# Optimization experiments

Hardware: AMD Instinct MI355X
Metric: run time of the kernel (lower is better)

The kernel has to match this reference:

```python
import jax, jax.numpy as jnp
import numpy as np

N = 10000
E = 160000
IN_DIM = 128
HID = 128
HEADS = 8
INT_DIM = 512
OUT_DIM = 3
NEG_SLOPE = 0.2


def gat_conv(x, src, dst, W, a_src, a_dst, b, heads, ch):
    # x: [N, F_in]; W: [F_in, heads*ch]; a_src/a_dst: [heads, ch]; b: [heads*ch]
    n = x.shape[0]
    h = (x @ W).reshape(n, heads, ch)                      # [N,H,C]
    alpha_src = jnp.einsum('nhc,hc->nh', h, a_src)         # [N,H]
    alpha_dst = jnp.einsum('nhc,hc->nh', h, a_dst)         # [N,H]
    e = jax.nn.leaky_relu(alpha_src[src] + alpha_dst[dst], NEG_SLOPE)  # [E,H]
    # segment softmax over incoming edges of each dst node
    emax = jax.ops.segment_max(e, dst, num_segments=n)     # [N,H]
    ee = jnp.exp(e - emax[dst])
    denom = jax.ops.segment_sum(ee, dst, num_segments=n)   # [N,H]
    alpha = ee / (denom[dst] + 1e-16)                      # [E,H]
    msg = h[src] * alpha[:, :, None]                       # [E,H,C]
    out = jax.ops.segment_sum(msg, dst, num_segments=n)    # [N,H,C]
    return out.reshape(n, heads * ch) + b


def setup_inputs() -> dict:
    key = jax.random.key(0)
    ks = jax.random.split(key, 20)

    def glorot(k, shape):
        fan = shape[0] + shape[-1]
        s = jnp.sqrt(6.0 / fan)
        return jax.random.uniform(k, shape, jnp.float32, -s, s)

    x = jax.random.normal(ks[0], (N, IN_DIM), jnp.float32)
    edge_index = jax.random.randint(ks[1], (2, E), 0, N, jnp.int32)
    return {
        'x': x,
        'edge_index': edge_index,
        'W1': glorot(ks[2], (IN_DIM, HEADS * HID)),
        'a_src1': glorot(ks[3], (HEADS, HID)),
        'a_dst1': glorot(ks[4], (HEADS, HID)),
        'b1': jnp.zeros((HEADS * HID,), jnp.float32),
        'W2': glorot(ks[5], (HEADS * HID, HEADS * HID)),
        'a_src2': glorot(ks[6], (HEADS, HID)),
        'a_dst2': glorot(ks[7], (HEADS, HID)),
        'b2': jnp.zeros((HEADS * HID,), jnp.float32),
        'W3': glorot(ks[8], (HEADS * HID, INT_DIM)),
        'a_src3': glorot(ks[9], (1, INT_DIM)),
        'a_dst3': glorot(ks[10], (1, INT_DIM)),
        'b3': jnp.zeros((INT_DIM,), jnp.float32),
        'Wl': glorot(ks[11], (INT_DIM, INT_DIM)),
        'bl': jnp.zeros((INT_DIM,), jnp.float32),
        'Wc': glorot(ks[12], (INT_DIM, OUT_DIM)),
        'bc': jnp.zeros((OUT_DIM,), jnp.float32),
    }


def reference(x, edge_index, W1, a_src1, a_dst1, b1, W2, a_src2, a_dst2, b2,
              W3, a_src3, a_dst3, b3, Wl, bl, Wc, bc):
    src, dst = edge_index[0], edge_index[1]
    # eval mode: dropout_edge and Dropout are identity
    h = gat_conv(x, src, dst, W1, a_src1, a_dst1, b1, HEADS, HID)
    h = jax.nn.relu(h)
    h = gat_conv(h, src, dst, W2, a_src2, a_dst2, b2, HEADS, HID)
    h = jax.nn.relu(h)
    h = gat_conv(h, src, dst, W3, a_src3, a_dst3, b3, 1, INT_DIM)
    h = jax.nn.relu(h)
    h = jax.nn.relu(h @ Wl + bl)
    return h @ Wc + bc
```

## Files before the change

kernel.cpp:

```cpp
#include <hip/hip_runtime.h>
#include <hip/hip_bf16.h>

#define NN 10000
#define EE 160000
#define IN_DIM 128
#define HID 128
#define HEADS 8
#define F1 (HEADS*HID)
#define INT_DIM 512
#define OUT_DIM 3
#define MPAD 10112

typedef __attribute__((ext_vector_type(4))) float f32x4;
typedef __attribute__((ext_vector_type(8))) _Float16 half8;
typedef __attribute__((ext_vector_type(4))) _Float16 half4;
typedef __attribute__((ext_vector_type(2))) _Float16 half2v;

#define WAVE_SYNC() do { asm volatile("s_waitcnt lgkmcnt(0)" ::: "memory"); \
                         __builtin_amdgcn_sched_barrier(0); } while(0)

#define FMA_MIX_LO(acc, pair, w) asm("v_fma_mix_f32 %0, %1, %2, %0 op_sel:[0,0,0] op_sel_hi:[1,0,0]" \
                                     : "+v"(acc) : "v"(pair), "v"(w))
#define FMA_MIX_HI(acc, pair, w) asm("v_fma_mix_f32 %0, %1, %2, %0 op_sel:[1,0,0] op_sel_hi:[1,0,0]" \
                                     : "+v"(acc) : "v"(pair), "v"(w))

__device__ inline void fma_mix8(float* acc, uint4 v, float w){
    FMA_MIX_LO(acc[0], v.x, w);  FMA_MIX_HI(acc[1], v.x, w);
    FMA_MIX_LO(acc[2], v.y, w);  FMA_MIX_HI(acc[3], v.y, w);
    FMA_MIX_LO(acc[4], v.z, w);  FMA_MIX_HI(acc[5], v.z, w);
    FMA_MIX_LO(acc[6], v.w, w);  FMA_MIX_HI(acc[7], v.w, w);
}

__global__ __launch_bounds__(1024) void scan_kernel(const int* __restrict__ cnt, int* __restrict__ rowp,
                                                    int* __restrict__ cursor, int n){
    int t = threadIdx.x;
    int base = t*10;
    int vals[10];
    int run = 0;
    #pragma unroll
    for(int k=0;k<10;k++){
        int i = base+k;
        int v = (i<n) ? cnt[i] : 0;
        vals[k] = run;
        run += v;
    }
    int lane = t & 63, wv = t >> 6;
    int inc = run;
    #pragma unroll
    for(int off=1; off<64; off<<=1){
        int u = __shfl_up(inc, off);
        if(lane >= off) inc += u;
    }
    __shared__ int wtot[16], woff[16];
    if(lane == 63) wtot[wv] = inc;
    __syncthreads();
    if(t < 16){
        int v = wtot[t];
        int inc2 = v;
        #pragma unroll
        for(int off=1; off<16; off<<=1){
            int u = __shfl_up(inc2, off);
            if(t >= off) inc2 += u;
        }
        woff[t] = inc2 - v;
    }
    __syncthreads();
    int thread_excl = woff[wv] + inc - run;
    #pragma unroll
    for(int k=0;k<10;k++){
        int i = base+k;
        if(i<n){
            int v = thread_excl + vals[k];
            rowp[i] = v;
            cursor[i] = v;
        }
    }
    if(t == 1023) rowp[n] = thread_excl + run;
}

__global__ __launch_bounds__(256) void fill_kernel(const int* __restrict__ src, const int* __restrict__ dst,
                                                   int E, int* __restrict__ cursor, int* __restrict__ colsrc){
    int e = blockIdx.x*256 + threadIdx.x;
    if(e < E){
        int d = dst[e];
        int pos = atomicAdd(&cursor[d], 1);
        colsrc[pos] = src[e];
    }
}

__device__ inline void transpose_tile16(const float* __restrict__ B, _Float16* __restrict__ T,
                                        int K, int N, int idx){
    __shared__ float tile[32][33];
    const int tx = threadIdx.x & 31, ty = threadIdx.x >> 5;
    const int gx = N >> 5;
    const int n0 = (idx % gx) * 32, k0 = (idx / gx) * 32;
    #pragma unroll
    for(int i = 0; i < 32; i += 8)
        tile[ty + i][tx] = B[(size_t)(k0 + ty + i) * N + n0 + tx];
    __syncthreads();
    #pragma unroll
    for(int i = 0; i < 32; i += 8){
        int nn = ty + i;
        T[(size_t)(n0 + nn) * K + k0 + tx] = (_Float16)tile[tx][nn];
    }
}

__global__ __launch_bounds__(256) void prep_kernel(
    const float* __restrict__ W1, const float* __restrict__ W2,
    const float* __restrict__ W3, const float* __restrict__ Wl,
    const float* __restrict__ x,
    const float* __restrict__ a_src1, const float* __restrict__ a_dst1,
    _Float16* __restrict__ tW1, _Float16* __restrict__ tW2,
    _Float16* __restrict__ tW3, _Float16* __restrict__ tWl,
    _Float16* __restrict__ x16, float* __restrict__ aw,
    int* __restrict__ cnt)
{
    int b = blockIdx.x;
    if(b < 128){            transpose_tile16(W1, tW1, IN_DIM, F1, b); }
    else if(b < 1152){      transpose_tile16(W2, tW2, F1, F1, b-128); }
    else if(b < 1664){      transpose_tile16(W3, tW3, F1, INT_DIM, b-1152); }
    else if(b < 1920){      transpose_tile16(Wl, tWl, INT_DIM, INT_DIM, b-1664); }
    else if(b < 3170){
        int i = (b-1920)*256 + threadIdx.x;
        float4 v = ((const float4*)x)[i];
        half4 o = { (_Float16)v.x, (_Float16)v.y, (_Float16)v.z, (_Float16)v.w };
        ((half4*)x16)[i] = o;
    }
    else if(b < 3178){
        int idx = (b-3170)*256 + threadIdx.x;
        if(idx < 16*IN_DIM){
            int j = idx >> 7, k = idx & 127;
            int hj = j & 7;
            const float* av = (j < 8 ? a_src1 : a_dst1) + hj*HID;
            const float* wr = W1 + (size_t)k*F1 + hj*HID;
            float s = 0.f;
            #pragma unroll 4
            for(int c = 0; c < HID; c++) s += av[c] * wr[c];
            aw[idx] = s;
        }
    }
    else {
        int i = (b-3178)*1024 + threadIdx.x*4;
        if(i < NN) *(int4*)(cnt + i) = (int4){0,0,0,0};
    }
}

__global__ __launch_bounds__(256) void count_alpha1_kernel(
    const int* __restrict__ dst, int* __restrict__ cnt,
    const float* __restrict__ x, const float* __restrict__ aw,
    float* __restrict__ asrc, float* __restrict__ adst)
{
    int b = blockIdx.x;
    if(b < 625){
        int e = b*256 + threadIdx.x;
        if(e < EE) atomicAdd(&cnt[dst[e]], 1);
        return;
    }
    __shared__ float xs[16][128];
    __shared__ float aws[16][128];
    int t = threadIdx.x;
    int nb = (b - 625) * 16;
    for(int i = t; i < 16*128; i += 256){
        xs[i >> 7][i & 127] = x[(size_t)nb*128 + i];
        aws[i >> 7][i & 127] = aw[i];
    }
    __syncthreads();
    int nl = t >> 4, j = t & 15;
    float s = 0.f;
    #pragma unroll 4
    for(int c = 0; c < 128; c++) s += xs[nl][c] * aws[j][c];
    int node = nb + nl;
    if(j < 8) asrc[node*8 + j] = s;
    else      adst[node*8 + (j-8)] = s;
}

__global__ __launch_bounds__(256) void agg1_kernel(const _Float16* __restrict__ x16,
                                                   const float* __restrict__ asrc,
                                                   const float* __restrict__ adst,
                                                   const int* __restrict__ rowp,
                                                   const int* __restrict__ colsrc,
                                                   _Float16* __restrict__ oa){
    const int w = threadIdx.x >> 6, l = threadIdx.x & 63;
    const int node = blockIdx.x*4 + w;
    __shared__ float sh_ee[4][64][8];
    int beg = rowp[node], end = rowp[node+1];
    float rd = adst[node*8 + (l & 7)];
    float acc0[8], acc1[8];
    #pragma unroll
    for(int h=0;h<8;h++){ acc0[h]=0.f; acc1[h]=0.f; }
    float dpart = 0.f;
    const char* xb = (const char*)x16 + 4*l;
    for(int base=beg; base<end; base+=64){
        int clen = min(64, end-base);
        WAVE_SYNC();
        unsigned soff = 0;
        if(l < clen) soff = (unsigned)colsrc[base + l] << 8;
        for(int it=l; it<clen*8; it+=64){
            int j = it >> 3;
            int s = colsrc[base + j];
            float e = asrc[s*8 + (l & 7)] + rd;
            e = (e > 0.f) ? e : 0.2f*e;
            float ee = expf(e);
            sh_ee[w][j][l & 7] = ee;
            dpart += ee;
        }
        WAVE_SYNC();
        #pragma unroll 2
        for(int j=0;j<clen;j++){
            unsigned o = (unsigned)__shfl((int)soff, j);
            unsigned pair = *(const unsigned*)(xb + o);
            #pragma unroll
            for(int h=0;h<8;h++){
                float wt = sh_ee[w][j][h];
                FMA_MIX_LO(acc0[h], pair, wt);
                FMA_MIX_HI(acc1[h], pair, wt);
            }
        }
    }
    dpart += __shfl_xor(dpart, 8);
    dpart += __shfl_xor(dpart, 16);
    dpart += __shfl_xor(dpart, 32);
    #pragma unroll
    for(int h=0;h<8;h++){
        float dn = __shfl(dpart, h) + 1e-16f;
        half2v o = { (_Float16)(acc0[h]/dn), (_Float16)(acc1[h]/dn) };
        *(half2v*)(oa + (size_t)node*F1 + h*128 + 2*l) = o;
    }
}

__device__ inline void agg_gather(const char* hb, unsigned soff, float ee, int clen,
                                  int g, uint4 v0, float w0, float* acc){
    int cpad = (clen + 3) & ~3;
    #pragma unroll 1
    for(int j0=0; j0<cpad; j0+=4){
        uint4 nv; float nw = 0.f;
        const bool more = (j0+4 < cpad);
        if(more){
            unsigned no = (unsigned)__shfl((int)soff, j0+4+g);
            nw = __shfl(ee, j0+4+g);
            nv = *(const uint4*)(hb + no);
        }
        fma_mix8(acc, v0, w0);
        if(more){ v0 = nv; w0 = nw; }
    }
}

__device__ inline void agg2_chunk(const char* hb, const float* asrc, const int* colsrc,
                                  int base, int clen, float rd, int h, int l, int g,
                                  float* acc, float& dpart){
    unsigned soff = 0; float eereg = 0.f;
    if(l < clen){
        int s = colsrc[base + l];
        soff = (unsigned)s << 11;
        float e = asrc[s*8 + h] + rd;
        e = (e > 0.f) ? e : 0.2f*e;
        eereg = expf(e);
        dpart += eereg;
    }
    unsigned o0 = (unsigned)__shfl((int)soff, g);
    float w0 = __shfl(eereg, g);
    uint4 v0 = *(const uint4*)(hb + o0);
    agg_gather(hb, soff, eereg, clen, g, v0, w0, acc);
}

__device__ inline void agg3_chunk(const char* hb, const float* asrc, const int* colsrc,
                                  int base, int clen, float rd, int l, int g,
                                  float* acc, float& dpart){
    unsigned soff = 0; float eereg = 0.f;
    if(l < clen){
        int s = colsrc[base + l];
        soff = (unsigned)s << 10;
        float e = asrc[s] + rd;
        e = (e > 0.f) ? e : 0.2f*e;
        eereg = expf(e);
        dpart += eereg;
    }
    unsigned o0 = (unsigned)__shfl((int)soff, g);
    float w0 = __shfl(eereg, g);
    uint4 v0 = *(const uint4*)(hb + o0);
    agg_gather(hb, soff, eereg, clen, g, v0, w0, acc);
}

__global__ __launch_bounds__(256) void agg2_kernel(const _Float16* __restrict__ hbuf,
                                                   const float* __restrict__ asrc,
                                                   const float* __restrict__ adst,
                                                   const int* __restrict__ rowp,
                                                   const int* __restrict__ colsrc,
                                                   const float* __restrict__ bias,
                                                   _Float16* __restrict__ oa){
    const int w = threadIdx.x >> 6, l = threadIdx.x & 63;
    const int h = blockIdx.x & 7;
    const int nA = (blockIdx.x >> 3)*8 + w*2;
    const int nB = nA + 1;
    const int g = l >> 4, i = l & 15;
    const char* hb = (const char*)hbuf + h*256 + 16*i;

    int begA = rowp[nA], endA = rowp[nA+1];
    int begB = rowp[nB], endB = rowp[nB+1];
    float rdA = adst[nA*8 + h];
    float rdB = adst[nB*8 + h];
    int clenA = min(64, endA - begA);
    int clenB = min(64, endB - begB);
    int sA = (l < clenA) ? colsrc[begA + l] : 0;
    int sB = (l < clenB) ? colsrc[begB + l] : 0;
    unsigned soffA = 0, soffB = 0;
    float eeA = 0.f, eeB = 0.f;
    if(l < clenA){
        soffA = (unsigned)sA << 11;
        float e = asrc[sA*8 + h] + rdA;
        e = (e > 0.f) ? e : 0.2f*e;
        eeA = expf(e);
    }
    if(l < clenB){
        soffB = (unsigned)sB << 11;
        float e = asrc[sB*8 + h] + rdB;
        e = (e > 0.f) ? e : 0.2f*e;
        eeB = expf(e);
    }
    unsigned oA = (unsigned)__shfl((int)soffA, g);
    float wA = __shfl(eeA, g);
    uint4 vA = *(const uint4*)(hb + oA);
    unsigned oB = (unsigned)__shfl((int)soffB, g);
    float wB = __shfl(eeB, g);
    uint4 vB = *(const uint4*)(hb + oB);

    float accA[8];
    #pragma unroll
    for(int k=0;k<8;k++) accA[k]=0.f;
    float dpA = eeA;
    agg_gather(hb, soffA, eeA, clenA, g, vA, wA, accA);
    for(int base=begA+64; base<endA; base+=64)
        agg2_chunk(hb, asrc, colsrc, base, min(64, endA-base), rdA, h, l, g, accA, dpA);

    float accB[8];
    #pragma unroll
    for(int k=0;k<8;k++) accB[k]=0.f;
    float dpB = eeB;
    agg_gather(hb, soffB, eeB, clenB, g, vB, wB, accB);
    for(int base=begB+64; base<endB; base+=64)
        agg2_chunk(hb, asrc, colsrc, base, min(64, endB-base), rdB, h, l, g, accB, dpB);

    #pragma unroll
    for(int k=0;k<8;k++){
        accA[k] += __shfl_xor(accA[k], 16);
        accA[k] += __shfl_xor(accA[k], 32);
        accB[k] += __shfl_xor(accB[k], 16);
        accB[k] += __shfl_xor(accB[k], 32);
    }
    #pragma unroll
    for(int off=1; off<64; off<<=1){
        dpA += __shfl_xor(dpA, off);
        dpB += __shfl_xor(dpB, off);
    }
    if(g == 0){
        const int f = h*128 + 8*i;
        float4 b0 = *(const float4*)(bias + f);
        float4 b1 = *(const float4*)(bias + f + 4);
        float bb[8] = {b0.x,b0.y,b0.z,b0.w, b1.x,b1.y,b1.z,b1.w};
        float dnA = dpA + 1e-16f, dnB = dpB + 1e-16f;
        half8 oA8, oB8;
        #pragma unroll
        for(int k=0;k<8;k++){
            oA8[k] = (_Float16)fmaxf(accA[k]/dnA + bb[k], 0.f);
            oB8[k] = (_Float16)fmaxf(accB[k]/dnB + bb[k], 0.f);
        }
        *(half8*)(oa + (size_t)nA*F1 + f) = oA8;
        *(half8*)(oa + (size_t)nB*F1 + f) = oB8;
    }
}

__global__ __launch_bounds__(256) void agg3_kernel(const _Float16* __restrict__ hbuf,
                                                   const float* __restrict__ asrc,
                                                   const float* __restrict__ adst,
                                                   const int* __restrict__ rowp,
                                                   const int* __restrict__ colsrc,
                                                   const float* __restrict__ bias,
                                                   _Float16* __restrict__ oa){
    const int w = threadIdx.x >> 6, l = threadIdx.x & 63;
    const int i7 = blockIdx.x & 7;
    const int chunk = i7 & 3, sub = i7 >> 2;
    const int nA = ((blockIdx.x >> 3)*2 + sub)*8 + w*2;
    const int nB = nA + 1;
    const int g = l >> 4, i = l & 15;
    const char* hb = (const char*)hbuf + chunk*256 + 16*i;

    int begA = rowp[nA], endA = rowp[nA+1];
    int begB = rowp[nB], endB = rowp[nB+1];
    float rdA = adst[nA];
    float rdB = adst[nB];
    int clenA = min(64, endA - begA);
    int clenB = min(64, endB - begB);
    int sA = (l < clenA) ? colsrc[begA + l] : 0;
    int sB = (l < clenB) ? colsrc[begB + l] : 0;
    unsigned soffA = 0, soffB = 0;
    float eeA = 0.f, eeB = 0.f;
    if(l < clenA){
        soffA = (unsigned)sA << 10;
        float e = asrc[sA] + rdA;
        e = (e > 0.f) ? e : 0.2f*e;
        eeA = expf(e);
    }
    if(l < clenB){
        soffB = (unsigned)sB << 10;
        float e = asrc[sB] + rdB;
        e = (e > 0.f) ? e : 0.2f*e;
        eeB = expf(e);
    }
    unsigned oA = (unsigned)__shfl((int)soffA, g);
    float wA = __shfl(eeA, g);
    uint4 vA = *(const uint4*)(hb + oA);
    unsigned oB = (unsigned)__shfl((int)soffB, g);
    float wB = __shfl(eeB, g);
    uint4 vB = *(const uint4*)(hb + oB);

    float accA[8];
    #pragma unroll
    for(int k=0;k<8;k++) accA[k]=0.f;
    float dpA = eeA;
    agg_gather(hb, soffA, eeA, clenA, g, vA, wA, accA);
    for(int base=begA+64; base<endA; base+=64)
        agg3_chunk(hb, asrc, colsrc, base, min(64, endA-base), rdA, l, g, accA, dpA);

    float accB[8];
    #pragma unroll
    for(int k=0;k<8;k++) accB[k]=0.f;
    float dpB = eeB;
    agg_gather(hb, soffB, eeB, clenB, g, vB, wB, accB);
    for(int base=begB+64; base<endB; base+=64)
        agg3_chunk(hb, asrc, colsrc, base, min(64, endB-base), rdB, l, g, accB, dpB);

    #pragma unroll
    for(int k=0;k<8;k++){
        accA[k] += __shfl_xor(accA[k], 16);
        accA[k] += __shfl_xor(accA[k], 32);
        accB[k] += __shfl_xor(accB[k], 16);
        accB[k] += __shfl_xor(accB[k], 32);
    }
    #pragma unroll
    for(int off=1; off<64; off<<=1){
        dpA += __shfl_xor(dpA, off);
        dpB += __shfl_xor(dpB, off);
    }
    if(g == 0){
        const int f = chunk*128 + 8*i;
        float4 b0 = *(const float4*)(bias + f);
        float4 b1 = *(const float4*)(bias + f + 4);
        float bb[8] = {b0.x,b0.y,b0.z,b0.w, b1.x,b1.y,b1.z,b1.w};
        float dnA = dpA + 1e-16f, dnB = dpB + 1e-16f;
        half8 oA8, oB8;
        #pragma unroll
        for(int k=0;k<8;k++){
            oA8[k] = (_Float16)fmaxf(accA[k]/dnA + bb[k], 0.f);
            oB8[k] = (_Float16)fmaxf(accB[k]/dnB + bb[k], 0.f);
        }
        *(half8*)(oa + (size_t)nA*INT_DIM + f) = oA8;
        *(half8*)(oa + (size_t)nB*INT_DIM + f) = oB8;
    }
}

template<int FUSE>
__global__ __launch_bounds__(512, 4) void mfma16_gemm_kernel(
    const _Float16* __restrict__ A, int lda, int za,
    const _Float16* __restrict__ B, int ldb, int zb,
    const float* __restrict__ bias, _Float16* __restrict__ O,
    int ldc, int zc, int K, int gx)
{
    __shared__ _Float16 lA[2][128*32];
    __shared__ _Float16 lB[2][128*32];
    const int tid  = threadIdx.x;
    const int lane = tid & 63;
    const int w    = tid >> 6;
    const int wm   = w >> 2;
    const int wn   = w & 3;
    const int z    = blockIdx.z;

    const int nwg = gridDim.x;
    const int q = nwg >> 3, r = nwg & 7;
    const int xcd = blockIdx.x & 7, idx = blockIdx.x >> 3;
    const int wgid = (xcd < r ? xcd*(q+1) : r*(q+1) + (xcd-r)*q) + idx;
    const int row0 = (wgid / gx) * 128, col0 = (wgid % gx) * 128;

    f32x4 acc[4][2];
    #pragma unroll
    for(int i=0;i<4;i++)
        #pragma unroll
        for(int j=0;j<2;j++) acc[i][j] = (f32x4){0.f,0.f,0.f,0.f};

    const int rr1 = tid >> 2;
    const int ss1 = (tid & 3) ^ ((rr1 >> 1) & 3);
    const size_t aoff = (size_t)(row0 + rr1) * lda + (size_t)z*za + ss1 * 8;
    const size_t boff = (size_t)(col0 + rr1) * ldb + (size_t)z*zb + ss1 * 8;

    typedef __attribute__((address_space(3))) char lds_char;
    lds_char* dA = (lds_char*)(&lA[0][0]) + w*1024;
    lds_char* dB = (lds_char*)(&lB[0][0]) + w*1024;

    int arow[4], brow[2];
    const int slotx = ((lane >> 4) ^ ((lane >> 1) & 3)) << 4;
    #pragma unroll
    for(int i=0;i<4;i++)
        arow[i] = (wm*64 + i*16 + (lane & 15)) * 64 + slotx;
    #pragma unroll
    for(int j=0;j<2;j++)
        brow[j] = (wn*32 + j*16 + (lane & 15)) * 64 + slotx;

    #define GLDS(src, dst) __builtin_amdgcn_global_load_lds( \
        (__attribute__((address_space(1))) void*)(src), \
        (__attribute__((address_space(3))) void*)(dst), 16, 0, 0)
    GLDS(A + aoff, dA);
    GLDS(B + boff, dB);
    __syncthreads();

    #pragma unroll 1
    for(int k0 = 0, kb = 0; k0 < K; k0 += 32, kb ^= 1){
        if(k0 + 32 < K){
            const int nb = kb ^ 1;
            GLDS(A + aoff + k0 + 32, dA + nb*8192);
            GLDS(B + boff + k0 + 32, dB + nb*8192);
        }
        const char* pA = (const char*)(&lA[0][0]) + kb*8192;
        const char* pB = (const char*)(&lB[0][0]) + kb*8192;
        half8 af[4];
        #pragma unroll
        for(int i=0;i<4;i++) af[i] = *(const half8*)(pA + arow[i]);
        #pragma unroll
        for(int j=0;j<2;j++){
            half8 bf = *(const half8*)(pB + brow[j]);
            #pragma unroll
            for(int i=0;i<4;i++)
                acc[i][j] = __builtin_amdgcn_mfma_f32_16x16x32_f16(af[i], bf, acc[i][j], 0, 0, 0);
        }
        __syncthreads();
    }
    #undef GLDS

    #pragma unroll
    for(int i=0;i<4;i++){
        const int rr = row0 + wm*64 + i*16 + ((lane >> 4) << 2);
        #pragma unroll
        for(int j=0;j<2;j++){
            const int gc = z*zc + col0 + wn*32 + j*16 + (lane & 15);
            float b = FUSE ? bias[gc] : 0.f;
            #pragma unroll
            for(int rg=0;rg<4;rg++){
                float v = acc[i][j][rg];
                if(FUSE) v = fmaxf(v + b, 0.f);
                O[(size_t)(rr + rg) * ldc + gc] = (_Float16)v;
            }
        }
    }
}

__global__ __launch_bounds__(128) void alpha16_h8_kernel(const _Float16* __restrict__ hbuf,
                                                         const float* __restrict__ a_src,
                                                         const float* __restrict__ a_dst,
                                                         float* __restrict__ asrc, float* __restrict__ adst){
    int node = blockIdx.x;
    int t = threadIdx.x;
    half8 v = ((const half8*)(hbuf + (size_t)node*F1))[t];
    const float4* ap = (const float4*)(a_src + 8*t);
    const float4* dp = (const float4*)(a_dst + 8*t);
    float4 a0 = ap[0], a1 = ap[1];
    float4 d0 = dp[0], d1 = dp[1];
    float av[8] = {a0.x,a0.y,a0.z,a0.w, a1.x,a1.y,a1.z,a1.w};
    float dv[8] = {d0.x,d0.y,d0.z,d0.w, d1.x,d1.y,d1.z,d1.w};
    float ps = 0.f, pd = 0.f;
    #pragma unroll
    for(int k=0;k<8;k++){
        float f = (float)v[k];
        ps += f * av[k];
        pd += f * dv[k];
    }
    #pragma unroll
    for(int off=8; off; off>>=1){ ps += __shfl_down(ps, off); pd += __shfl_down(pd, off); }
    if((t & 15) == 0){
        asrc[(size_t)node*8 + (t>>4)] = ps;
        adst[(size_t)node*8 + (t>>4)] = pd;
    }
}

__global__ __launch_bounds__(128) void alpha16_h1_kernel(const _Float16* __restrict__ hbuf,
                                                         const float* __restrict__ a_src,
                                                         const float* __restrict__ a_dst,
                                                         float* __restrict__ asrc, float* __restrict__ adst){
    int node = blockIdx.x;
    int t = threadIdx.x;
    half4 v = ((const half4*)(hbuf + (size_t)node*INT_DIM))[t];
    float4 a = ((const float4*)a_src)[t];
    float4 d = ((const float4*)a_dst)[t];
    float ps = (float)v[0]*a.x + (float)v[1]*a.y + (float)v[2]*a.z + (float)v[3]*a.w;
    float pd = (float)v[0]*d.x + (float)v[1]*d.y + (float)v[2]*d.z + (float)v[3]*d.w;
    #pragma unroll
    for(int off=32; off; off>>=1){ ps += __shfl_down(ps, off); pd += __shfl_down(pd, off); }
    __shared__ float shs[2], shd[2];
    int wv = t >> 6;
    if((t & 63) == 0){ shs[wv] = ps; shd[wv] = pd; }
    __syncthreads();
    if(t == 0){
        asrc[node] = shs[0] + shs[1];
        adst[node] = shd[0] + shd[1];
    }
}

__global__ __launch_bounds__(256) void cls16_kernel(const _Float16* __restrict__ h, const float* __restrict__ Wc,
                                                    const float* __restrict__ bc, float* __restrict__ out, int n){
    int node = blockIdx.x*4 + (threadIdx.x >> 6);
    int lane = threadIdx.x & 63;
    if(node >= n) return;
    half8 v = ((const half8*)(h + (size_t)node*INT_DIM))[lane];
    float s0=0.f, s1=0.f, s2=0.f;
    #pragma unroll
    for(int k=0;k<8;k++){
        float f = (float)v[k];
        const float* wr = Wc + (8*lane + k)*3;
        s0 += f * wr[0];
        s1 += f * wr[1];
        s2 += f * wr[2];
    }
    #pragma unroll
    for(int off=32; off; off>>=1){
        s0 += __shfl_down(s0, off);
        s1 += __shfl_down(s1, off);
        s2 += __shfl_down(s2, off);
    }
    if(lane==0){
        out[(size_t)node*3+0] = s0 + bc[0];
        out[(size_t)node*3+1] = s1 + bc[1];
        out[(size_t)node*3+2] = s2 + bc[2];
    }
}

extern "C" void kernel_launch(void* const* d_in, const int* in_sizes, int n_in,
                              void* d_out, int out_size, void* d_ws, size_t ws_size,
                              hipStream_t stream){
    const float* x      = (const float*)d_in[0];
    const int*   ei     = (const int*)d_in[1];
    const float* W1     = (const float*)d_in[2];
    const float* a_src1 = (const float*)d_in[3];
    const float* a_dst1 = (const float*)d_in[4];
    const float* b1     = (const float*)d_in[5];
    const float* W2     = (const float*)d_in[6];
    const float* a_src2 = (const float*)d_in[7];
    const float* a_dst2 = (const float*)d_in[8];
    const float* b2     = (const float*)d_in[9];
    const float* W3     = (const float*)d_in[10];
    const float* a_src3 = (const float*)d_in[11];
    const float* a_dst3 = (const float*)d_in[12];
    const float* b3     = (const float*)d_in[13];
    const float* Wl     = (const float*)d_in[14];
    const float* bl     = (const float*)d_in[15];
    const float* Wc     = (const float*)d_in[16];
    const float* bc     = (const float*)d_in[17];
    float* out = (float*)d_out;

    const int* src = ei;
    const int* dst = ei + EE;

    char* p = (char*)d_ws;
    char* regA = p;  p += (size_t)MPAD*F1*4;
    char* regB = p;  p += (size_t)MPAD*F1*4;
    float* aw1  = (float*)p;  p += 16*IN_DIM*4;
    float* asrc = (float*)p;  p += (size_t)NN*HEADS*4;
    float* adst = (float*)p;  p += (size_t)NN*HEADS*4;
    int* cnt    = (int*)p;    p += NN*4;
    int* rowp   = (int*)p;    p += (NN+1)*4;
    int* cursor = (int*)p;    p += NN*4;
    int* colsrc = (int*)p;    p += EE*4;

    _Float16* hA = (_Float16*)regA;
    _Float16* hB = (_Float16*)regB;
    _Float16* up   = (_Float16*)(regA + (size_t)MPAD*F1*2);
    _Float16* tW1  = up;
    _Float16* tW2  = tW1 + (size_t)F1*IN_DIM;
    _Float16* tW3  = tW2 + (size_t)F1*F1;
    _Float16* tWl  = tW3 + (size_t)INT_DIM*F1;
    _Float16* x16  = tWl + (size_t)INT_DIM*INT_DIM;

    prep_kernel<<<3188, 256, 0, stream>>>(W1, W2, W3, Wl, x, a_src1, a_dst1,
                                          tW1, tW2, tW3, tWl, x16, aw1, cnt);
    count_alpha1_kernel<<<1250, 256, 0, stream>>>(dst, cnt, x, aw1, asrc, adst);
    scan_kernel<<<1, 1024, 0, stream>>>(cnt, rowp, cursor, NN);
    fill_kernel<<<(EE+255)/256, 256, 0, stream>>>(src, dst, EE, cursor, colsrc);

    agg1_kernel<<<NN/4, 256, 0, stream>>>(x16, asrc, adst, rowp, colsrc, hA);
    mfma16_gemm_kernel<1><<<dim3(MPAD/128, 1, HEADS), 512, 0, stream>>>(
        hA, F1, 128,  tW1, IN_DIM, 128*IN_DIM,
        b1, hB, F1, 128,  IN_DIM, 1);

    mfma16_gemm_kernel<0><<<dim3((F1/128)*(MPAD/128), 1, 1), 512, 0, stream>>>(
        hB, F1, 0,  tW2, F1, 0,
        nullptr, hA, F1, 0,  F1, F1/128);
    alpha16_h8_kernel<<<NN, 128, 0, stream>>>(hA, a_src2, a_dst2, asrc, adst);
    agg2_kernel<<<(NN/8)*8, 256, 0, stream>>>(hA, asrc, adst, rowp, colsrc, b2, hB);

    mfma16_gemm_kernel<0><<<dim3((INT_DIM/128)*(MPAD/128), 1, 1), 512, 0, stream>>>(
        hB, F1, 0,  tW3, F1, 0,
        nullptr, hA, INT_DIM, 0,  F1, INT_DIM/128);
    alpha16_h1_kernel<<<NN, 128, 0, stream>>>(hA, a_src3, a_dst3, asrc, adst);
    agg3_kernel<<<(NN/16)*8, 256, 0, stream>>>(hA, asrc, adst, rowp, colsrc, b3, hB);

    mfma16_gemm_kernel<1><<<dim3((INT_DIM/128)*(MPAD/128), 1, 1), 512, 0, stream>>>(
        hB, INT_DIM, 0,  tWl, INT_DIM, 0,
        bl, hA, INT_DIM, 0,  INT_DIM, INT_DIM/128);

    cls16_kernel<<<(NN+3)/4, 256, 0, stream>>>(hA, Wc, bc, out, NN);
}
```

Measured before the change: 247.1 us.

## Rotate per-node head chunks in GEMM output to spread aggregation gathers across channels

The layer-2 and layer-3 GEMMs now write each node's 128-column head or chunk groups rotated by the node index. The alpha and aggregation kernels read through the same permutation. Concurrent blocks for the same head therefore touch different 256-byte offsets within rows, which should spread gather traffic across memory channels and banks and reduce hot-spotting. It adds a few integer ops per address and couples the producer and consumer layouts, so any mismatch would silently corrupt results.

```diff
diff --git a/kernel.cpp b/kernel.cpp
--- a/kernel.cpp
+++ b/kernel.cpp
@@ -251,7 +251,7 @@
     unsigned soff = 0; float eereg = 0.f;
     if(l < clen){
         int s = colsrc[base + l];
-        soff = (unsigned)s << 11;
+        soff = ((unsigned)s << 11) | ((unsigned)((h + s) & 7) << 8);
         float e = asrc[s*8 + h] + rd;
         e = (e > 0.f) ? e : 0.2f*e;
         eereg = expf(e);
@@ -264,12 +264,12 @@
 }
 
 __device__ inline void agg3_chunk(const char* hb, const float* asrc, const int* colsrc,
-                                  int base, int clen, float rd, int l, int g,
+                                  int base, int clen, float rd, int chunk, int l, int g,
                                   float* acc, float& dpart){
     unsigned soff = 0; float eereg = 0.f;
     if(l < clen){
         int s = colsrc[base + l];
-        soff = (unsigned)s << 10;
+        soff = ((unsigned)s << 10) | ((unsigned)((chunk + s) & 3) << 8);
         float e = asrc[s] + rd;
         e = (e > 0.f) ? e : 0.2f*e;
         eereg = expf(e);
@@ -293,7 +293,7 @@
     const int nA = (blockIdx.x >> 3)*8 + w*2;
     const int nB = nA + 1;
     const int g = l >> 4, i = l & 15;
-    const char* hb = (const char*)hbuf + h*256 + 16*i;
+    const char* hb = (const char*)hbuf + 16*i;
 
     int begA = rowp[nA], endA = rowp[nA+1];
     int begB = rowp[nB], endB = rowp[nB+1];
@@ -306,13 +306,13 @@
     unsigned soffA = 0, soffB = 0;
     float eeA = 0.f, eeB = 0.f;
     if(l < clenA){
-        soffA = (unsigned)sA << 11;
+        soffA = ((unsigned)sA << 11) | ((unsigned)((h + sA) & 7) << 8);
         float e = asrc[sA*8 + h] + rdA;
         e = (e > 0.f) ? e : 0.2f*e;
         eeA = expf(e);
     }
     if(l < clenB){
-        soffB = (unsigned)sB << 11;
+        soffB = ((unsigned)sB << 11) | ((unsigned)((h + sB) & 7) << 8);
         float e = asrc[sB*8 + h] + rdB;
         e = (e > 0.f) ? e : 0.2f*e;
         eeB = expf(e);
@@ -382,7 +382,7 @@
     const int nA = ((blockIdx.x >> 3)*2 + sub)*8 + w*2;
     const int nB = nA + 1;
     const int g = l >> 4, i = l & 15;
-    const char* hb = (const char*)hbuf + chunk*256 + 16*i;
+    const char* hb = (const char*)hbuf + 16*i;
 
     int begA = rowp[nA], endA = rowp[nA+1];
     int begB = rowp[nB], endB = rowp[nB+1];
@@ -395,13 +395,13 @@
     unsigned soffA = 0, soffB = 0;
     float eeA = 0.f, eeB = 0.f;
     if(l < clenA){
-        soffA = (unsigned)sA << 10;
+        soffA = ((unsigned)sA << 10) | ((unsigned)((chunk + sA) & 3) << 8);
         float e = asrc[sA] + rdA;
         e = (e > 0.f) ? e : 0.2f*e;
         eeA = expf(e);
     }
     if(l < clenB){
-        soffB = (unsigned)sB << 10;
+        soffB = ((unsigned)sB << 10) | ((unsigned)((chunk + sB) & 3) << 8);
         float e = asrc[sB] + rdB;
         e = (e > 0.f) ? e : 0.2f*e;
         eeB = expf(e);
@@ -419,7 +419,7 @@
     float dpA = eeA;
     agg_gather(hb, soffA, eeA, clenA, g, vA, wA, accA);
     for(int base=begA+64; base<endA; base+=64)
-        agg3_chunk(hb, asrc, colsrc, base, min(64, endA-base), rdA, l, g, accA, dpA);
+        agg3_chunk(hb, asrc, colsrc, base, min(64, endA-base), rdA, chunk, l, g, accA, dpA);
 
     float accB[8];
     #pragma unroll
@@ -427,7 +427,7 @@
     float dpB = eeB;
     agg_gather(hb, soffB, eeB, clenB, g, vB, wB, accB);
     for(int base=begB+64; base<endB; base+=64)
-        agg3_chunk(hb, asrc, colsrc, base, min(64, endB-base), rdB, l, g, accB, dpB);
+        agg3_chunk(hb, asrc, colsrc, base, min(64, endB-base), rdB, chunk, l, g, accB, dpB);
 
     #pragma unroll
     for(int k=0;k<8;k++){
@@ -458,7 +458,7 @@
     }
 }
 
-template<int FUSE>
+template<int FUSE, int ROTM>
 __global__ __launch_bounds__(512, 4) void mfma16_gemm_kernel(
     const _Float16* __restrict__ A, int lda, int za,
     const _Float16* __restrict__ B, int ldb, int zb,
@@ -545,7 +545,13 @@
             for(int rg=0;rg<4;rg++){
                 float v = acc[i][j][rg];
                 if(FUSE) v = fmaxf(v + b, 0.f);
-                O[(size_t)(rr + rg) * ldc + gc] = (_Float16)v;
+                const int node = rr + rg;
+                int pc = gc;
+                if(ROTM){
+                    int grp = ((gc >> 7) + node) & ROTM;
+                    pc = (gc & 127) | (grp << 7);
+                }
+                O[(size_t)node * ldc + pc] = (_Float16)v;
             }
         }
     }
@@ -557,7 +563,9 @@
                                                          float* __restrict__ asrc, float* __restrict__ adst){
     int node = blockIdx.x;
     int t = threadIdx.x;
-    half8 v = ((const half8*)(hbuf + (size_t)node*F1))[t];
+    int head = t >> 4;
+    int poff = (((head + node) & 7) << 7) + ((t & 15) << 3);
+    half8 v = *(const half8*)(hbuf + (size_t)node*F1 + poff);
     const float4* ap = (const float4*)(a_src + 8*t);
     const float4* dp = (const float4*)(a_dst + 8*t);
     float4 a0 = ap[0], a1 = ap[1];
@@ -574,8 +582,8 @@
     #pragma unroll
     for(int off=8; off; off>>=1){ ps += __shfl_down(ps, off); pd += __shfl_down(pd, off); }
     if((t & 15) == 0){
-        asrc[(size_t)node*8 + (t>>4)] = ps;
-        adst[(size_t)node*8 + (t>>4)] = pd;
+        asrc[(size_t)node*8 + head] = ps;
+        adst[(size_t)node*8 + head] = pd;
     }
 }
 
@@ -585,7 +593,9 @@
                                                          float* __restrict__ asrc, float* __restrict__ adst){
     int node = blockIdx.x;
     int t = threadIdx.x;
-    half4 v = ((const half4*)(hbuf + (size_t)node*INT_DIM))[t];
+    int chunk = t >> 5;
+    int poff = (((chunk + node) & 3) << 7) + ((t & 31) << 2);
+    half4 v = *(const half4*)(hbuf + (size_t)node*INT_DIM + poff);
     float4 a = ((const float4*)a_src)[t];
     float4 d = ((const float4*)a_dst)[t];
     float ps = (float)v[0]*a.x + (float)v[1]*a.y + (float)v[2]*a.z + (float)v[3]*a.w;
@@ -683,23 +693,23 @@
     fill_kernel<<<(EE+255)/256, 256, 0, stream>>>(src, dst, EE, cursor, colsrc);
 
     agg1_kernel<<<NN/4, 256, 0, stream>>>(x16, asrc, adst, rowp, colsrc, hA);
-    mfma16_gemm_kernel<1><<<dim3(MPAD/128, 1, HEADS), 512, 0, stream>>>(
+    mfma16_gemm_kernel<1,0><<<dim3(MPAD/128, 1, HEADS), 512, 0, stream>>>(
         hA, F1, 128,  tW1, IN_DIM, 128*IN_DIM,
         b1, hB, F1, 128,  IN_DIM, 1);
 
-    mfma16_gemm_kernel<0><<<dim3((F1/128)*(MPAD/128), 1, 1), 512, 0, stream>>>(
+    mfma16_gemm_kernel<0,7><<<dim3((F1/128)*(MPAD/128), 1, 1), 512, 0, stream>>>(
         hB, F1, 0,  tW2, F1, 0,
         nullptr, hA, F1, 0,  F1, F1/128);
     alpha16_h8_kernel<<<NN, 128, 0, stream>>>(hA, a_src2, a_dst2, asrc, adst);
     agg2_kernel<<<(NN/8)*8, 256, 0, stream>>>(hA, asrc, adst, rowp, colsrc, b2, hB);
 
-    mfma16_gemm_kernel<0><<<dim3((INT_DIM/128)*(MPAD/128), 1, 1), 512, 0, stream>>>(
+    mfma16_gemm_kernel<0,3><<<dim3((INT_DIM/128)*(MPAD/128), 1, 1), 512, 0, stream>>>(
         hB, F1, 0,  tW3, F1, 0,
         nullptr, hA, INT_DIM, 0,  F1, INT_DIM/128);
     alpha16_h1_kernel<<<NN, 128, 0, stream>>>(hA, a_src3, a_dst3, asrc, adst);
     agg3_kernel<<<(NN/16)*8, 256, 0, stream>>>(hA, asrc, adst, rowp, colsrc, b3, hB);
 
-    mfma16_gemm_kernel<1><<<dim3((INT_DIM/128)*(MPAD/128), 1, 1), 512, 0, stream>>>(
+    mfma16_gemm_kernel<1,0><<<dim3((INT_DIM/128)*(MPAD/128), 1, 1), 512, 0, stream>>>(
         hB, INT_DIM, 0,  tWl, INT_DIM, 0,
         bl, hA, INT_DIM, 0,  INT_DIM, INT_DIM/128);
 
```

New measurement: 250.1 us. No clear change (+1.2%).
